# Kernel tuning notes

Hardware: AMD Instinct MI355X
Metric: run time of the kernel (lower is better)

The kernel has to match this reference:

```python
import jax, jax.numpy as jnp
import numpy as np

B, N, H, DR = 4, 512, 512, 64  # batch, nodes, hidden_size, d_relation
ALPHA = 1.0
EPS = 1e-5  # nn.LayerNorm default


def setup_inputs() -> dict:
    key = jax.random.key(0)
    ks = jax.random.split(key, 16)
    def g(k, shape, s=0.02):
        return jax.random.normal(k, shape, jnp.float32) * s
    return {
        'node': jax.random.normal(ks[0], (B, N, H), jnp.float32),
        'node_mass': jax.random.normal(ks[1], (B, N, DR), jnp.float32),
        'dist': jax.random.randint(ks[2], (B, N, N), 0, 100),
        'predecessors': jax.random.randint(ks[3], (B, N, N, 1), 0, N),
        'rel_mask': jnp.ones((B, N, N, 1), dtype=bool),
        'Wq': g(ks[4], (DR, H)), 'bq': jnp.zeros((DR,), jnp.float32),
        'Wk': g(ks[5], (DR, H)), 'bk': jnp.zeros((DR,), jnp.float32),
        'Wp': g(ks[6], (DR, H)), 'bp': jnp.zeros((DR,), jnp.float32),
        'Wv': g(ks[7], (H, H)), 'bv': jnp.zeros((H,), jnp.float32),
        'dist_emb': g(ks[8], (100, DR)),
        'Wt': g(ks[9], (DR, DR)),
        'Wo': g(ks[10], (H, H)), 'bo': jnp.zeros((H,), jnp.float32),
        'pred_pad': jax.random.normal(ks[11], (DR,), jnp.float32),
        'ln_g': jnp.ones((H,), jnp.float32),
        'ln_b': jnp.zeros((H,), jnp.float32),
    }


def apply_rope(x, dis):
    # dis: [B,N,DR] -> sin/cos halves [B,N,DR/2]
    sin, cos = jnp.split(dis, 2, axis=-1)
    x0, x1 = x[..., 0::2], x[..., 1::2]
    return jnp.concatenate([x0 * cos - x1 * sin, x1 * cos + x0 * sin], axis=-1)


def reference(node, node_mass, dist, predecessors, rel_mask,
              Wq, bq, Wk, bk, Wp, bp, Wv, bv, dist_emb, Wt, Wo, bo,
              pred_pad, ln_g, ln_b):
    q = apply_rope(node @ Wq.T + bq, node_mass)          # [B,N,DR]
    k = apply_rope(node @ Wk.T + bk, node_mass)          # [B,N,DR]
    p = node @ Wp.T + bp                                  # [B,N,DR]

    idx = predecessors[..., 0]                            # [B,N,N] int
    # gather: pred_g[b,n,m,:] = p[b, idx[b,n,m], :]
    pred_g = jax.vmap(lambda pb, ib: pb[ib])(p, idx)      # [B,N,N,DR]
    pmask = (idx == 0)[..., None]                         # [B,N,N,1]
    pred_g = jnp.where(pmask, pred_pad, pred_g)

    rel = jnp.einsum('bni,bmi->bnmi', q, k) + dist_emb[dist] + pred_g  # [B,N,N,DR]
    rel = rel @ Wt.T                                      # talking heads
    rel = jnp.where(rel_mask, rel, -jnp.inf)
    rel = jax.nn.softmax(rel, axis=-2)                    # softmax over m

    v = (node @ Wv.T + bv).reshape(B, N, DR, H // DR)     # [B,N,DR,H/DR]
    post = jnp.einsum('bnmi,bmij->bnij', rel, v).reshape(B, N, H)
    post = post @ Wo.T + bo

    x = node * ALPHA + post                               # DeepNorm (dropout=0)
    mu = jnp.mean(x, axis=-1, keepdims=True)
    var = jnp.var(x, axis=-1, keepdims=True)
    return (x - mu) / jnp.sqrt(var + EPS) * ln_g + ln_b
```

## Files before the change

kernel.cpp:

```cpp
#include <hip/hip_runtime.h>
#include <hip/hip_bf16.h>

typedef unsigned short u16;
typedef __attribute__((ext_vector_type(8))) short short8;
typedef __attribute__((ext_vector_type(4))) short short4b;
typedef __attribute__((ext_vector_type(8))) unsigned short ushort8;
typedef __attribute__((ext_vector_type(4))) unsigned short ush4;
typedef __attribute__((ext_vector_type(2))) unsigned short ush2;
typedef __attribute__((ext_vector_type(4))) float f32x4;
typedef __attribute__((ext_vector_type(4))) int i32x4;

__device__ __forceinline__ float b2f(u16 u) {
    union { unsigned int i; float f; } x; x.i = ((unsigned int)u) << 16; return x.f;
}
__device__ __forceinline__ u16 f2b(float f) {
    union { float f; unsigned int i; } x; x.f = f;
    unsigned int r = x.i + 0x7FFFu + ((x.i >> 16) & 1u);
    return (u16)(r >> 16);
}
__device__ __forceinline__ unsigned int pack2(float a, float b) {
    union { float f; unsigned int u; } x, y; x.f = a; y.f = b;
    return (x.u >> 16) | (y.u & 0xFFFF0000u);
}

__global__ __launch_bounds__(256) void kprep2(
    const float* __restrict__ dist_emb, const float* __restrict__ Wt,
    const float* __restrict__ pred_pad, const float* __restrict__ bp,
    const float* __restrict__ Wp, const float* __restrict__ Wo,
    const int* __restrict__ dist, const int* __restrict__ pred,
    float* __restrict__ embTT, float* __restrict__ padT,
    float* __restrict__ bpT, float* __restrict__ Wtp,
    u16* __restrict__ WoB, u16* __restrict__ packT)
{
    __shared__ u16 tile[64][65];
    int bx = blockIdx.x;
    int t = threadIdx.x;
    if (bx >= 282) {
        int pb = bx - 282;
        int ntb = pb & 7, mtb = (pb >> 3) & 7, b = pb >> 6;
        int r = t >> 2, c0 = (t & 3) * 16;
        size_t base = ((size_t)(b * 512 + ntb * 64 + r)) * 512 + mtb * 64 + c0;
        #pragma unroll
        for (int cq = 0; cq < 4; ++cq) {
            i32x4 dv = *reinterpret_cast<const i32x4*>(dist + base + cq * 4);
            i32x4 xv = *reinterpret_cast<const i32x4*>(pred + base + cq * 4);
            #pragma unroll
            for (int e = 0; e < 4; ++e)
                tile[c0 + cq * 4 + e][r] = (u16)(dv[e] | (xv[e] << 7));
        }
        __syncthreads();
        size_t orow = ((size_t)(b * 512 + mtb * 64 + r)) * 512 + ntb * 64;
        int q = t & 3;
        #pragma unroll
        for (int z = 0; z < 16; ++z) {
            int op = q * 16 + z;
            int wg = op & 31;
            int c = (op & 32) + ((wg & 1) << 4) + (wg >> 1);
            packT[orow + op] = tile[r][c];
        }
        return;
    }
    int u = bx * 256 + t;
    if (u < 6400) {
        int d = u >> 6, j = u & 63;
        float s = 0.f;
        #pragma unroll 8
        for (int i = 0; i < 64; ++i) s += dist_emb[d*64+i] * Wt[j*64+i];
        embTT[j*100 + d] = s;
    } else if (u < 6528) {
        int j = u - 6400;
        if (j < 64) {
            float s = 0.f;
            for (int i = 0; i < 64; ++i) s += pred_pad[i] * Wt[j*64+i];
            padT[j] = s;
        } else {
            int jj = j - 64;
            float s = 0.f;
            for (int i = 0; i < 64; ++i) s += bp[i] * Wt[jj*64+i];
            bpT[jj] = s;
        }
    } else if (u < 6528 + 32768) {
        int w = u - 6528;
        int row = w >> 9, h = w & 511;
        float s = 0.f;
        #pragma unroll 8
        for (int i = 0; i < 64; ++i) s += Wt[row*64+i] * Wp[i*512+h];
        Wtp[(size_t)row * 512 + h] = s;
    } else if (u < 6528 + 32768 + 32768) {
        int w = u - (6528 + 32768);
        int row = w >> 6, cu = (w & 63) * 8;
        const float* src = Wo + (size_t)row * 512 + cu;
        ushort8 o;
        #pragma unroll
        for (int e = 0; e < 8; ++e) o[e] = f2b(src[e]);
        *reinterpret_cast<ushort8*>(&WoB[(size_t)row * 512 + cu]) = o;
    }
}

__global__ __launch_bounds__(256) void kg1(
    const float* __restrict__ node, const float* __restrict__ Wq,
    const float* __restrict__ Wk, const float* __restrict__ Wtp,
    const float* __restrict__ Wv,
    const float* __restrict__ node_mass, const float* __restrict__ bq,
    const float* __restrict__ bk, const float* __restrict__ bpT,
    const float* __restrict__ bv,
    float* __restrict__ qf, u16* __restrict__ kf,
    float* __restrict__ pTT, u16* __restrict__ vbT)
{
    __shared__ __align__(16) char smem[18432];
    u16* As = (u16*)smem;
    u16* Bs = As + 64 * 72;
    int t = threadIdx.x;
    int lane = t & 63, lo = lane & 15, hi = lane >> 4, w = t >> 6;
    int M0 = blockIdx.x * 64;
    int y = blockIdx.y;
    int wm = w >> 1, wn = w & 1;

    const float* bsrc;
    if (y == 0)      bsrc = Wq;
    else if (y == 1) bsrc = Wk;
    else if (y == 2) bsrc = Wtp;
    else             bsrc = Wv + (size_t)(y - 3) * 64 * 512;

    f32x4 acc[2][2];
    #pragma unroll
    for (int fr = 0; fr < 2; ++fr)
        #pragma unroll
        for (int fc = 0; fc < 2; ++fc) acc[fr][fc] = (f32x4){0.f, 0.f, 0.f, 0.f};

    for (int kc = 0; kc < 512; kc += 64) {
        #pragma unroll
        for (int p = 0; p < 2; ++p) {
            int ua = t + p * 256;
            int row = ua >> 3, cu = (ua & 7) * 8;
            const float* ap = node + (size_t)(M0 + row) * 512 + kc + cu;
            f32x4 a0 = *reinterpret_cast<const f32x4*>(ap);
            f32x4 a1 = *reinterpret_cast<const f32x4*>(ap + 4);
            const float* bp_ = bsrc + (size_t)row * 512 + kc + cu;
            f32x4 b0 = *reinterpret_cast<const f32x4*>(bp_);
            f32x4 b1 = *reinterpret_cast<const f32x4*>(bp_ + 4);
            ushort8 oa, ob;
            #pragma unroll
            for (int e = 0; e < 4; ++e) {
                oa[e] = f2b(a0[e]); oa[4 + e] = f2b(a1[e]);
                ob[e] = f2b(b0[e]); ob[4 + e] = f2b(b1[e]);
            }
            *reinterpret_cast<ushort8*>(&As[row * 72 + cu]) = oa;
            *reinterpret_cast<ushort8*>(&Bs[row * 72 + cu]) = ob;
        }
        __syncthreads();
        #pragma unroll
        for (int ks = 0; ks < 2; ++ks) {
            short8 a0 = *reinterpret_cast<const short8*>(&As[(wm*32 + lo)      * 72 + ks*32 + hi*8]);
            short8 a1 = *reinterpret_cast<const short8*>(&As[(wm*32 + 16 + lo) * 72 + ks*32 + hi*8]);
            short8 b0 = *reinterpret_cast<const short8*>(&Bs[(wn*32 + lo)      * 72 + ks*32 + hi*8]);
            short8 b1 = *reinterpret_cast<const short8*>(&Bs[(wn*32 + 16 + lo) * 72 + ks*32 + hi*8]);
            acc[0][0] = __builtin_amdgcn_mfma_f32_16x16x32_bf16(a0, b0, acc[0][0], 0, 0, 0);
            acc[0][1] = __builtin_amdgcn_mfma_f32_16x16x32_bf16(a0, b1, acc[0][1], 0, 0, 0);
            acc[1][0] = __builtin_amdgcn_mfma_f32_16x16x32_bf16(a1, b0, acc[1][0], 0, 0, 0);
            acc[1][1] = __builtin_amdgcn_mfma_f32_16x16x32_bf16(a1, b1, acc[1][1], 0, 0, 0);
        }
        __syncthreads();
    }

    int b = M0 >> 9;
    if (y <= 1) {
        const float* bias = (y == 0) ? bq : bk;
        #pragma unroll
        for (int fr = 0; fr < 2; ++fr)
            #pragma unroll
            for (int fc = 0; fc < 2; ++fc) {
                int o = wn * 32 + fc * 16 + lo;
                float bb = bias[o];
                #pragma unroll
                for (int e = 0; e < 4; ++e) {
                    int r = M0 + wm * 32 + fr * 16 + hi * 4 + e;
                    float x = acc[fr][fc][e] + bb;
                    float xp = __shfl_xor(x, 1);
                    int uu = o >> 1;
                    float sv = node_mass[(size_t)r * 64 + uu];
                    float cv = node_mass[(size_t)r * 64 + 32 + uu];
                    if (o & 1) {
                        float val = x * cv + xp * sv;
                        if (y == 0) qf[(size_t)r * 64 + 32 + uu] = val;
                        else        kf[(size_t)r * 64 + 32 + uu] = f2b(val);
                    } else {
                        float val = x * cv - xp * sv;
                        if (y == 0) qf[(size_t)r * 64 + uu] = val;
                        else        kf[(size_t)r * 64 + uu] = f2b(val);
                    }
                }
            }
    } else if (y == 2) {
        float* ft = (float*)smem;
        __syncthreads();
        #pragma unroll
        for (int fr = 0; fr < 2; ++fr)
            #pragma unroll
            for (int fc = 0; fc < 2; ++fc) {
                int c = wn * 32 + fc * 16 + lo;
                float bb = bpT[c];
                #pragma unroll
                for (int e = 0; e < 4; ++e) {
                    int rl = wm * 32 + fr * 16 + hi * 4 + e;
                    ft[rl * 65 + c] = acc[fr][fc][e] + bb;
                }
            }
        __syncthreads();
        int o = t >> 2, seg = t & 3;
        int nbase = (M0 & 511) + seg * 16;
        float* dst = pTT + ((size_t)b * 64 + o) * 512 + nbase;
        #pragma unroll
        for (int g = 0; g < 4; ++g) {
            f32x4 v;
            #pragma unroll
            for (int i = 0; i < 4; ++i) v[i] = ft[(seg * 16 + g * 4 + i) * 65 + o];
            *reinterpret_cast<f32x4*>(dst + g * 4) = v;
        }
    } else {
        #pragma unroll
        for (int fr = 0; fr < 2; ++fr)
            #pragma unroll
            for (int fc = 0; fc < 2; ++fc) {
                int o = (y - 3) * 64 + wn * 32 + fc * 16 + lo;
                float bb = bv[o];
                int ii = o >> 3, jj = o & 7;
                #pragma unroll
                for (int e = 0; e < 4; ++e) {
                    int r = M0 + wm * 32 + fr * 16 + hi * 4 + e;
                    int n = r & 511;
                    vbT[(((size_t)b * 64 + ii) * 512 + n) * 8 + jj] = f2b(acc[fr][fc][e] + bb);
                }
            }
    }
}

__global__ __launch_bounds__(512, 4) void k2_attn(
    const float* __restrict__ qf, const u16* __restrict__ kf,
    const float* __restrict__ pTT, const u16* __restrict__ vbT,
    const float* __restrict__ embTT, const float* __restrict__ padT,
    const u16* __restrict__ packT, const float* __restrict__ Wt,
    u16* __restrict__ postB)
{
    __shared__ u16   Ai[32 * 72];
    __shared__ u16   vT[16 * 520];
    __shared__ float etab[104];
    __shared__ float ptab[512];
    __shared__ float maxb[8 * 32];
    __shared__ float sumb[8 * 32];
    __shared__ float pvred[8 * 256];

    int t = threadIdx.x;
    int lane = t & 63, lo = lane & 15, hi = lane >> 4, wave = t >> 6;
    int idx = blockIdx.x;
    int i    = idx & 63;
    int nt16 = (idx >> 6) & 15;
    int b    = idx >> 10;
    int n0   = nt16 * 32;

    if (t < 100) etab[t] = embTT[i * 100 + t];
    ptab[t] = (t == 0) ? padT[i] : pTT[((size_t)b * 64 + i) * 512 + t];
    {
        ushort8 vv = *reinterpret_cast<const ushort8*>(
            vbT + (((size_t)b * 64 + i) * 512 + t) * 8);
        #pragma unroll
        for (int j = 0; j < 8; ++j) vT[j * 520 + t] = vv[j];
        for (int u = t; u < 8 * 520; u += 512) vT[8 * 520 + u] = 0;
    }
    {
        int r = t >> 4, c0 = (t & 15) * 4;
        const float* qrow = qf + ((size_t)(b * 512 + n0 + r)) * 64 + c0;
        const float* wrow = Wt + i * 64 + c0;
        ush4 o;
        #pragma unroll
        for (int e = 0; e < 4; ++e) o[e] = f2b(qrow[e] * wrow[e]);
        *reinterpret_cast<ush4*>(&Ai[r * 72 + c0]) = o;
    }
    __syncthreads();

    f32x4 acc[4][2];
    #pragma unroll
    for (int mt = 0; mt < 4; ++mt) {
        const u16* ab = kf + (size_t)(b * 512 + wave * 64 + mt * 16 + lo) * 64 + hi * 8;
        short8 A0 = *reinterpret_cast<const short8*>(ab);
        short8 A1 = *reinterpret_cast<const short8*>(ab + 32);
        #pragma unroll
        for (int nt = 0; nt < 2; ++nt) {
            short8 Bf0 = *reinterpret_cast<const short8*>(&Ai[(nt * 16 + lo) * 72 + hi * 8]);
            short8 Bf1 = *reinterpret_cast<const short8*>(&Ai[(nt * 16 + lo) * 72 + 32 + hi * 8]);
            f32x4 a = (f32x4){0.f, 0.f, 0.f, 0.f};
            a = __builtin_amdgcn_mfma_f32_16x16x32_bf16(A0, Bf0, a, 0, 0, 0);
            a = __builtin_amdgcn_mfma_f32_16x16x32_bf16(A1, Bf1, a, 0, 0, 0);
            acc[mt][nt] = a;
        }
    }

    #pragma unroll
    for (int mt = 0; mt < 4; ++mt) {
        ush2 codes[4];
        #pragma unroll
        for (int e = 0; e < 4; ++e) {
            int m = wave * 64 + mt * 16 + hi * 4 + e;
            codes[e] = *reinterpret_cast<const ush2*>(
                &packT[((size_t)(b * 512 + m)) * 512 + n0 + lo * 2]);
        }
        #pragma unroll
        for (int e = 0; e < 4; ++e)
            #pragma unroll
            for (int nt = 0; nt < 2; ++nt) {
                unsigned int pc = codes[e][nt];
                acc[mt][nt][e] += etab[pc & 127u] + ptab[pc >> 7];
            }
    }

    float M[2];
    #pragma unroll
    for (int nt = 0; nt < 2; ++nt) {
        float mx = acc[0][nt][0];
        #pragma unroll
        for (int mt = 0; mt < 4; ++mt)
            #pragma unroll
            for (int e = 0; e < 4; ++e) mx = fmaxf(mx, acc[mt][nt][e]);
        mx = fmaxf(mx, __shfl_xor(mx, 16));
        mx = fmaxf(mx, __shfl_xor(mx, 32));
        if (lane < 16) maxb[wave * 32 + nt * 16 + lo] = mx;
    }
    __syncthreads();
    #pragma unroll
    for (int nt = 0; nt < 2; ++nt) {
        int c = nt * 16 + lo;
        float mm = maxb[c];
        #pragma unroll
        for (int w = 1; w < 8; ++w) mm = fmaxf(mm, maxb[w * 32 + c]);
        M[nt] = mm;
    }

    unsigned int pk[4][2][2];
    float Ssum[2] = {0.f, 0.f};
    #pragma unroll
    for (int mt = 0; mt < 4; ++mt) {
        #pragma unroll
        for (int nt = 0; nt < 2; ++nt) {
            float e0 = __expf(acc[mt][nt][0] - M[nt]);
            float e1 = __expf(acc[mt][nt][1] - M[nt]);
            float e2 = __expf(acc[mt][nt][2] - M[nt]);
            float e3 = __expf(acc[mt][nt][3] - M[nt]);
            Ssum[nt] += (e0 + e1) + (e2 + e3);
            pk[mt][nt][0] = pack2(e0, e1);
            pk[mt][nt][1] = pack2(e2, e3);
        }
    }
    #pragma unroll
    for (int nt = 0; nt < 2; ++nt) {
        float s = Ssum[nt];
        s += __shfl_xor(s, 16);
        s += __shfl_xor(s, 32);
        if (lane < 16) sumb[wave * 32 + nt * 16 + lo] = s;
    }

    f32x4 pvacc[2];
    #pragma unroll
    for (int nt = 0; nt < 2; ++nt) pvacc[nt] = (f32x4){0.f, 0.f, 0.f, 0.f};
    #pragma unroll
    for (int mp = 0; mp < 2; ++mp) {
        int base = wave * 64 + mp * 32;
        union { short4b s[2]; short8 s8; } bv;
        bv.s[0] = *reinterpret_cast<const short4b*>(&vT[lo * 520 + base + hi * 4]);
        bv.s[1] = *reinterpret_cast<const short4b*>(&vT[lo * 520 + base + 16 + hi * 4]);
        #pragma unroll
        for (int nt = 0; nt < 2; ++nt) {
            union { unsigned int u[4]; short8 s; } av;
            av.u[0] = pk[2*mp][nt][0];
            av.u[1] = pk[2*mp][nt][1];
            av.u[2] = pk[2*mp+1][nt][0];
            av.u[3] = pk[2*mp+1][nt][1];
            pvacc[nt] = __builtin_amdgcn_mfma_f32_16x16x32_bf16(av.s, bv.s8, pvacc[nt], 0, 0, 0);
        }
    }

    if (lo < 8) {
        #pragma unroll
        for (int nt = 0; nt < 2; ++nt)
            #pragma unroll
            for (int e = 0; e < 4; ++e)
                pvred[wave * 256 + (nt * 16 + hi * 4 + e) * 8 + lo] = pvacc[nt][e];
    }
    __syncthreads();
    if (t < 256) {
        int n = t >> 3, j = t & 7;
        float s = 0.f, L = 0.f;
        #pragma unroll
        for (int w = 0; w < 8; ++w) {
            s += pvred[w * 256 + n * 8 + j];
            L += sumb[w * 32 + n];
        }
        postB[((size_t)(b * 512 + n0 + n)) * 512 + i * 8 + j] = f2b(s / L);
    }
}

__global__ __launch_bounds__(512) void kout(
    const u16* __restrict__ postB, const u16* __restrict__ WoB,
    const float* __restrict__ node, const float* __restrict__ bo,
    const float* __restrict__ ln_g, const float* __restrict__ ln_b,
    float* __restrict__ out)
{
    __shared__ u16 As[16 * 520];
    __shared__ float part[8][16][2];
    __shared__ float musig[16][2];
    int t = threadIdx.x, lane = t & 63, lo = lane & 15, hi = lane >> 4, w = t >> 6;
    int row0 = blockIdx.x * 8;

    {
        int r = t >> 6, cu = (t & 63) * 8;
        *reinterpret_cast<ushort8*>(&As[r * 520 + cu]) =
            *reinterpret_cast<const ushort8*>(&postB[(size_t)(row0 + r) * 512 + cu]);
        *reinterpret_cast<ushort8*>(&As[(8 + r) * 520 + cu]) =
            (ushort8){0, 0, 0, 0, 0, 0, 0, 0};
    }
    __syncthreads();

    f32x4 acc[4];
    #pragma unroll
    for (int ct = 0; ct < 4; ++ct) acc[ct] = (f32x4){0.f, 0.f, 0.f, 0.f};
    for (int kc = 0; kc < 512; kc += 32) {
        short8 A0 = *reinterpret_cast<const short8*>(&As[lo * 520 + kc + hi * 8]);
        #pragma unroll
        for (int ct = 0; ct < 4; ++ct) {
            int col = w * 64 + ct * 16 + lo;
            short8 B0 = *reinterpret_cast<const short8*>(&WoB[(size_t)col * 512 + kc + hi * 8]);
            acc[ct] = __builtin_amdgcn_mfma_f32_16x16x32_bf16(A0, B0, acc[ct], 0, 0, 0);
        }
    }

    float xv[4][4];
    float sum_[4] = {0.f, 0.f, 0.f, 0.f}, ssq_[4] = {0.f, 0.f, 0.f, 0.f};
    #pragma unroll
    for (int ct = 0; ct < 4; ++ct) {
        int col = w * 64 + ct * 16 + lo;
        float bb = bo[col];
        #pragma unroll
        for (int e = 0; e < 4; ++e) {
            int row = hi * 4 + e;
            float x = acc[ct][e] + bb + node[(size_t)(row0 + (row & 7)) * 512 + col];
            xv[ct][e] = x;
            sum_[e] += x; ssq_[e] += x * x;
        }
    }
    #pragma unroll
    for (int e = 0; e < 4; ++e) {
        #pragma unroll
        for (int off = 1; off < 16; off <<= 1) {
            sum_[e] += __shfl_xor(sum_[e], off);
            ssq_[e] += __shfl_xor(ssq_[e], off);
        }
    }
    if (lo == 0) {
        #pragma unroll
        for (int e = 0; e < 4; ++e) {
            part[w][hi * 4 + e][0] = sum_[e];
            part[w][hi * 4 + e][1] = ssq_[e];
        }
    }
    __syncthreads();
    if (t < 16) {
        float s = 0.f, q = 0.f;
        #pragma unroll
        for (int ww = 0; ww < 8; ++ww) { s += part[ww][t][0]; q += part[ww][t][1]; }
        float mu = s * (1.f / 512.f);
        float var = q * (1.f / 512.f) - mu * mu;
        musig[t][0] = mu;
        musig[t][1] = rsqrtf(var + 1e-5f);
    }
    __syncthreads();
    if (hi < 2) {
        #pragma unroll
        for (int ct = 0; ct < 4; ++ct) {
            int col = w * 64 + ct * 16 + lo;
            float g = ln_g[col], bb = ln_b[col];
            #pragma unroll
            for (int e = 0; e < 4; ++e) {
                int row = hi * 4 + e;
                float mu = musig[row][0], rs = musig[row][1];
                out[(size_t)(row0 + row) * 512 + col] = (xv[ct][e] - mu) * rs * g + bb;
            }
        }
    }
}

extern "C" void kernel_launch(void* const* d_in, const int* in_sizes, int n_in,
                              void* d_out, int out_size, void* d_ws, size_t ws_size,
                              hipStream_t stream)
{
    const float* node      = (const float*)d_in[0];
    const float* node_mass = (const float*)d_in[1];
    const int*   dist      = (const int*)d_in[2];
    const int*   pred      = (const int*)d_in[3];
    const float* Wq = (const float*)d_in[5];
    const float* bq = (const float*)d_in[6];
    const float* Wk = (const float*)d_in[7];
    const float* bk = (const float*)d_in[8];
    const float* Wp = (const float*)d_in[9];
    const float* bp = (const float*)d_in[10];
    const float* Wv = (const float*)d_in[11];
    const float* bv = (const float*)d_in[12];
    const float* dist_emb = (const float*)d_in[13];
    const float* Wt = (const float*)d_in[14];
    const float* Wo = (const float*)d_in[15];
    const float* bo = (const float*)d_in[16];
    const float* pred_pad = (const float*)d_in[17];
    const float* ln_g = (const float*)d_in[18];
    const float* ln_b = (const float*)d_in[19];

    char* ws = (char*)d_ws;
    float* qf    = (float*)(ws + 0);
    u16*   kf    = (u16*)  (ws + 524288);
    float* pTT   = (float*)(ws + 786432);
    u16*   vbT   = (u16*)  (ws + 1310720);
    u16*   postB = (u16*)  (ws + 3407872);
    float* embTT = (float*)(ws + 5505024);
    float* padT  = (float*)(ws + 5530624);
    float* bpT   = (float*)(ws + 5530880);
    float* Wtp   = (float*)(ws + 5531136);
    u16*   WoB   = (u16*)  (ws + 5662208);
    u16*   packT = (u16*)  (ws + 6186496);

    kprep2<<<538, 256, 0, stream>>>(dist_emb, Wt, pred_pad, bp, Wp, Wo,
                                    dist, pred, embTT, padT, bpT, Wtp, WoB, packT);
    kg1<<<dim3(32, 11), 256, 0, stream>>>(node, Wq, Wk, Wtp, Wv, node_mass,
                                          bq, bk, bpT, bv, qf, kf, pTT, vbT);
    k2_attn<<<4096, 512, 0, stream>>>(qf, kf, pTT, vbT, embTT, padT, packT, Wt, postB);
    kout<<<256, 512, 0, stream>>>(postB, WoB, node, bo, ln_g, ln_b, (float*)d_out);
}
```

Baseline: 109.1 us.

## Move dist/pred packing into projection kernel and use full 16-row tiles in output GEMM

The dist/predecessor pack-and-transpose work moves out of the prep kernel into an extra blockIdx.y slice of the projection GEMM kernel. Each of its 32 blocks now processes 8 tiles in a loop, where before there was one tile per block. Separately, the output projection + LayerNorm kernel now fills all 16 MFMA rows with real data instead of padding 8 with zeros, halving its grid to 128 blocks. The first change shortens the prep kernel's critical path but serializes packing inside fewer blocks. The second removes wasted MFMA work and halves the number of Wo reads per row, at the cost of fewer blocks than CUs.

```diff
diff --git a/kernel.cpp b/kernel.cpp
--- a/kernel.cpp
+++ b/kernel.cpp
@@ -23,44 +23,15 @@
     return (x.u >> 16) | (y.u & 0xFFFF0000u);
 }
 
-__global__ __launch_bounds__(256) void kprep2(
+__global__ __launch_bounds__(256) void kprep(
     const float* __restrict__ dist_emb, const float* __restrict__ Wt,
     const float* __restrict__ pred_pad, const float* __restrict__ bp,
     const float* __restrict__ Wp, const float* __restrict__ Wo,
-    const int* __restrict__ dist, const int* __restrict__ pred,
     float* __restrict__ embTT, float* __restrict__ padT,
     float* __restrict__ bpT, float* __restrict__ Wtp,
-    u16* __restrict__ WoB, u16* __restrict__ packT)
+    u16* __restrict__ WoB)
 {
-    __shared__ u16 tile[64][65];
-    int bx = blockIdx.x;
-    int t = threadIdx.x;
-    if (bx >= 282) {
-        int pb = bx - 282;
-        int ntb = pb & 7, mtb = (pb >> 3) & 7, b = pb >> 6;
-        int r = t >> 2, c0 = (t & 3) * 16;
-        size_t base = ((size_t)(b * 512 + ntb * 64 + r)) * 512 + mtb * 64 + c0;
-        #pragma unroll
-        for (int cq = 0; cq < 4; ++cq) {
-            i32x4 dv = *reinterpret_cast<const i32x4*>(dist + base + cq * 4);
-            i32x4 xv = *reinterpret_cast<const i32x4*>(pred + base + cq * 4);
-            #pragma unroll
-            for (int e = 0; e < 4; ++e)
-                tile[c0 + cq * 4 + e][r] = (u16)(dv[e] | (xv[e] << 7));
-        }
-        __syncthreads();
-        size_t orow = ((size_t)(b * 512 + mtb * 64 + r)) * 512 + ntb * 64;
-        int q = t & 3;
-        #pragma unroll
-        for (int z = 0; z < 16; ++z) {
-            int op = q * 16 + z;
-            int wg = op & 31;
-            int c = (op & 32) + ((wg & 1) << 4) + (wg >> 1);
-            packT[orow + op] = tile[r][c];
-        }
-        return;
-    }
-    int u = bx * 256 + t;
+    int u = blockIdx.x * 256 + threadIdx.x;
     if (u < 6400) {
         int d = u >> 6, j = u & 63;
         float s = 0.f;
@@ -104,16 +75,49 @@
     const float* __restrict__ node_mass, const float* __restrict__ bq,
     const float* __restrict__ bk, const float* __restrict__ bpT,
     const float* __restrict__ bv,
+    const int* __restrict__ dist, const int* __restrict__ pred,
     float* __restrict__ qf, u16* __restrict__ kf,
-    float* __restrict__ pTT, u16* __restrict__ vbT)
+    float* __restrict__ pTT, u16* __restrict__ vbT,
+    u16* __restrict__ packT)
 {
     __shared__ __align__(16) char smem[18432];
+    int t = threadIdx.x;
+    int y = blockIdx.y;
+
+    if (y == 11) {
+        u16* tile = (u16*)smem;
+        int x = blockIdx.x;
+        for (int pb = x * 8; pb < x * 8 + 8; ++pb) {
+            int ntb = pb & 7, mtb = (pb >> 3) & 7, b = pb >> 6;
+            int r = t >> 2, c0 = (t & 3) * 16;
+            size_t base = ((size_t)(b * 512 + ntb * 64 + r)) * 512 + mtb * 64 + c0;
+            #pragma unroll
+            for (int cq = 0; cq < 4; ++cq) {
+                i32x4 dv = *reinterpret_cast<const i32x4*>(dist + base + cq * 4);
+                i32x4 xv = *reinterpret_cast<const i32x4*>(pred + base + cq * 4);
+                #pragma unroll
+                for (int e = 0; e < 4; ++e)
+                    tile[(c0 + cq * 4 + e) * 65 + r] = (u16)(dv[e] | (xv[e] << 7));
+            }
+            __syncthreads();
+            size_t orow = ((size_t)(b * 512 + mtb * 64 + r)) * 512 + ntb * 64;
+            int q = t & 3;
+            #pragma unroll
+            for (int z = 0; z < 16; ++z) {
+                int op = q * 16 + z;
+                int wg = op & 31;
+                int c = (op & 32) + ((wg & 1) << 4) + (wg >> 1);
+                packT[orow + op] = tile[r * 65 + c];
+            }
+            __syncthreads();
+        }
+        return;
+    }
+
     u16* As = (u16*)smem;
     u16* Bs = As + 64 * 72;
-    int t = threadIdx.x;
     int lane = t & 63, lo = lane & 15, hi = lane >> 4, w = t >> 6;
     int M0 = blockIdx.x * 64;
-    int y = blockIdx.y;
     int wm = w >> 1, wn = w & 1;
 
     const float* bsrc;
@@ -408,14 +412,14 @@
     __shared__ float part[8][16][2];
     __shared__ float musig[16][2];
     int t = threadIdx.x, lane = t & 63, lo = lane & 15, hi = lane >> 4, w = t >> 6;
-    int row0 = blockIdx.x * 8;
-
-    {
-        int r = t >> 6, cu = (t & 63) * 8;
+    int row0 = blockIdx.x * 16;
+
+    #pragma unroll
+    for (int p = 0; p < 2; ++p) {
+        int u = t + p * 512;
+        int r = u >> 6, cu = (u & 63) * 8;
         *reinterpret_cast<ushort8*>(&As[r * 520 + cu]) =
             *reinterpret_cast<const ushort8*>(&postB[(size_t)(row0 + r) * 512 + cu]);
-        *reinterpret_cast<ushort8*>(&As[(8 + r) * 520 + cu]) =
-            (ushort8){0, 0, 0, 0, 0, 0, 0, 0};
     }
     __syncthreads();
 
@@ -441,7 +445,7 @@
         #pragma unroll
         for (int e = 0; e < 4; ++e) {
             int row = hi * 4 + e;
-            float x = acc[ct][e] + bb + node[(size_t)(row0 + (row & 7)) * 512 + col];
+            float x = acc[ct][e] + bb + node[(size_t)(row0 + row) * 512 + col];
             xv[ct][e] = x;
             sum_[e] += x; ssq_[e] += x * x;
         }
@@ -472,17 +476,15 @@
         musig[t][1] = rsqrtf(var + 1e-5f);
     }
     __syncthreads();
-    if (hi < 2) {
-        #pragma unroll
-        for (int ct = 0; ct < 4; ++ct) {
-            int col = w * 64 + ct * 16 + lo;
-            float g = ln_g[col], bb = ln_b[col];
-            #pragma unroll
-            for (int e = 0; e < 4; ++e) {
-                int row = hi * 4 + e;
-                float mu = musig[row][0], rs = musig[row][1];
-                out[(size_t)(row0 + row) * 512 + col] = (xv[ct][e] - mu) * rs * g + bb;
-            }
+    #pragma unroll
+    for (int ct = 0; ct < 4; ++ct) {
+        int col = w * 64 + ct * 16 + lo;
+        float g = ln_g[col], bb = ln_b[col];
+        #pragma unroll
+        for (int e = 0; e < 4; ++e) {
+            int row = hi * 4 + e;
+            float mu = musig[row][0], rs = musig[row][1];
+            out[(size_t)(row0 + row) * 512 + col] = (xv[ct][e] - mu) * rs * g + bb;
         }
     }
 }
@@ -524,10 +526,11 @@
     u16*   WoB   = (u16*)  (ws + 5662208);
     u16*   packT = (u16*)  (ws + 6186496);
 
-    kprep2<<<538, 256, 0, stream>>>(dist_emb, Wt, pred_pad, bp, Wp, Wo,
-                                    dist, pred, embTT, padT, bpT, Wtp, WoB, packT);
-    kg1<<<dim3(32, 11), 256, 0, stream>>>(node, Wq, Wk, Wtp, Wv, node_mass,
-                                          bq, bk, bpT, bv, qf, kf, pTT, vbT);
+    kprep<<<282, 256, 0, stream>>>(dist_emb, Wt, pred_pad, bp, Wp, Wo,
+                                   embTT, padT, bpT, Wtp, WoB);
+    kg1<<<dim3(32, 12), 256, 0, stream>>>(node, Wq, Wk, Wtp, Wv, node_mass,
+                                          bq, bk, bpT, bv, dist, pred,
+                                          qf, kf, pTT, vbT, packT);
     k2_attn<<<4096, 512, 0, stream>>>(qf, kf, pTT, vbT, embTT, padT, packT, Wt, postB);
-    kout<<<256, 512, 0, stream>>>(postB, WoB, node, bo, ln_g, ln_b, (float*)d_out);
-}
+    kout<<<128, 512, 0, stream>>>(postB, WoB, node, bo, ln_g, ln_b, (float*)d_out);
+}
```

New measurement: 109.0 us (median of 2 runs). No clear change (-0.0%).
